# Kernel tuning notes

Measured on AMD Instinct MI355X. Metric: run time of the kernel, lower is better.

Reference implementation:

```python
import jax, jax.numpy as jnp
import numpy as np

N_NODES = 100_000
N_EDGES = 1_600_000
F_IN = 32
F_OUT = 32
DIM = 2
K = 5                      # kernel_size per dim (open spline)
KTOT = K ** DIM            # 25 kernel weight matrices
S = 2 ** DIM               # 4 nonzero linear-B-spline basis terms per edge
NEG_SLOPE = 0.2

# offsets over the 2^DIM corners of the spline cell, [S, DIM]
_OFFSETS = np.array([[(s >> d) & 1 for d in range(DIM)] for s in range(S)], dtype=np.int32)
_STRIDES = np.array([K ** d for d in range(DIM)], dtype=np.int32)


def _spline_basis(pseudo):
    """Degree-1 open B-spline basis. pseudo: [E, DIM] in [0,1].
    Returns basis [E, S] and kernel-weight indices widx [E, S]."""
    offsets = jnp.asarray(_OFFSETS)
    strides = jnp.asarray(_STRIDES)
    p = pseudo * (K - 1)                         # open spline scaling
    fl = jnp.floor(p)
    frac = p - fl                                # [E, DIM]
    b = jnp.where(offsets[None] == 0, 1.0 - frac[:, None, :], frac[:, None, :])
    basis = jnp.prod(b, axis=-1)                 # [E, S]
    idx = jnp.clip(fl.astype(jnp.int32)[:, None, :] + offsets[None], 0, K - 1)
    widx = jnp.sum(idx * strides, axis=-1)       # [E, S] in [0, KTOT)
    return basis, widx


def setup_inputs() -> dict:
    key = jax.random.key(0)
    ks = jax.random.split(key, 7)
    x = jax.random.normal(ks[0], (N_NODES, F_IN), dtype=jnp.float32)
    edge_index = jax.random.randint(ks[1], (2, N_EDGES), 0, N_NODES)
    pseudo = jax.random.uniform(ks[2], (N_EDGES, DIM), dtype=jnp.float32)
    bound = 1.0 / np.sqrt(KTOT * F_IN)           # matches reset_parameters uniform(size, ...)
    weight = jax.random.uniform(ks[3], (KTOT, F_IN, F_OUT), jnp.float32, -bound, bound)
    root_weight = jax.random.uniform(ks[4], (F_IN, F_OUT), jnp.float32, -bound, bound)
    att_weight = jax.random.uniform(ks[5], (2 * F_OUT,), jnp.float32, -bound, bound)
    bias = jax.random.uniform(ks[6], (F_OUT,), jnp.float32, -bound, bound)
    return {"x": x, "edge_index": edge_index, "pseudo": pseudo, "weight": weight,
            "root_weight": root_weight, "att_weight": att_weight, "bias": bias}


def reference(x, edge_index, pseudo, weight, root_weight, att_weight, bias):
    row, col = edge_index[0], edge_index[1]      # row = target, col = source
    basis, widx = _spline_basis(pseudo)          # [E,S], [E,S]

    # Precompute x @ W_k for every kernel weight: [N, KTOT, F_OUT]
    xw = jnp.einsum('nf,kfo->nko', x, weight)
    flat = col[:, None] * KTOT + widx            # [E, S] flat (node, kernel) index
    gathered = xw.reshape(-1, F_OUT)[flat]       # [E, S, F_OUT]
    msg = jnp.einsum('es,esf->ef', basis, gathered)  # spline-weighted edge messages

    x_root = x @ root_weight                     # [N, F_OUT]

    # GAT-style attention logits: cat([x_root[row], msg]) . att_weight
    alpha = x_root[row] @ att_weight[:F_OUT] + msg @ att_weight[F_OUT:]
    alpha = jnp.where(alpha > 0, alpha, NEG_SLOPE * alpha)  # leaky relu

    # segment softmax over incoming edges of each target node
    amax = jax.ops.segment_max(alpha, row, num_segments=N_NODES)
    amax = jnp.where(jnp.isfinite(amax), amax, 0.0)
    ex = jnp.exp(alpha - amax[row])
    denom = jax.ops.segment_sum(ex, row, num_segments=N_NODES)
    att = ex / (denom[row] + 1e-16)

    out = jax.ops.segment_sum(msg * att[:, None], row, num_segments=N_NODES)
    return out + x_root + bias
```

## Files before the change

### kernel.cpp

```cpp
#include <hip/hip_runtime.h>
#include <stdint.h>

#define N_NODES 100000
#define N_EDGES 1600000
#define NBLK_SCAN 391

typedef __attribute__((ext_vector_type(8))) short short8;
typedef __attribute__((ext_vector_type(4))) float float4v;

__device__ __forceinline__ unsigned short f32_to_bf16(float f) {
  uint32_t u = __float_as_uint(f);
  u += 0x7fffu + ((u >> 16) & 1u);
  return (unsigned short)(u >> 16);
}
__device__ __forceinline__ float bf16_to_f32(unsigned short h) {
  return __uint_as_float(((uint32_t)h) << 16);
}

__global__ __launch_bounds__(256) void k_zero(
    const float* __restrict__ weight, const float* __restrict__ root_w,
    int* __restrict__ deg, unsigned short* __restrict__ wbf) {
  int tid = threadIdx.x;
  int b = blockIdx.x;
  int i = b * 256 + tid;
  if (i < N_NODES) deg[i] = 0;
  if (b < 100) {
    int e = i;
    int t = e >> 9, rem = e & 511;
    int q = rem >> 7, row = (rem >> 3) & 15, j = rem & 7;
    int km = t >> 1, fin = q * 8 + j, fo = (t & 1) * 16 + row;
    wbf[e] = f32_to_bf16(weight[(km * 32 + fin) * 32 + fo]);
  } else if (b == 100) {
    for (int idx = tid; idx < 1024; idx += 256) {
      int t = 50 + (idx >> 9), rem = idx & 511;
      int q = rem >> 7, row = (rem >> 3) & 15, j = rem & 7;
      int fin = q * 8 + j, fo = (t - 50) * 16 + row;
      wbf[t * 512 + rem] = f32_to_bf16(root_w[fin * 32 + fo]);
    }
  }
}

__global__ __launch_bounds__(256) void k1_xw(
    const float* __restrict__ x, const unsigned short* __restrict__ wbf,
    const int* __restrict__ ei, const float* __restrict__ att_w,
    const float* __restrict__ bias,
    int* __restrict__ deg, unsigned short* __restrict__ rank,
    unsigned short* __restrict__ xw, float* __restrict__ out,
    uint2* __restrict__ od) {
  __shared__ __align__(16) uint2 st[3200];
  int tid = threadIdx.x;
  int b = blockIdx.x;

  int e = b * 256 + tid;
  int rk = atomicAdd(&deg[ei[e]], 1);

  int wave = tid >> 6, lane = tid & 63;
  int quad = lane >> 4, c16 = lane & 15;
  int n0 = b * 16;
  int node = n0 + c16;
  const float* xp = x + (size_t)node * 32 + quad * 8;
  float4 a0 = *reinterpret_cast<const float4*>(xp);
  float4 a1 = *reinterpret_cast<const float4*>(xp + 4);
  short8 af;
  af[0] = (short)f32_to_bf16(a0.x); af[1] = (short)f32_to_bf16(a0.y);
  af[2] = (short)f32_to_bf16(a0.z); af[3] = (short)f32_to_bf16(a0.w);
  af[4] = (short)f32_to_bf16(a1.x); af[5] = (short)f32_to_bf16(a1.y);
  af[6] = (short)f32_to_bf16(a1.z); af[7] = (short)f32_to_bf16(a1.w);

  float rsum = 0.f;
  for (int idx = 0; idx < 13; idx++) {
    int t = wave * 13 + idx;
    short8 bf = *reinterpret_cast<const short8*>(wbf + ((t * 4 + quad) * 16 + c16) * 8);
    float4v acc = {0.f, 0.f, 0.f, 0.f};
    acc = __builtin_amdgcn_mfma_f32_16x16x32_bf16(bf, af, acc, 0, 0, 0);
    if (t < 50) {
      uint2 pk;
      pk.x = (unsigned int)f32_to_bf16(acc[0]) |
             ((unsigned int)f32_to_bf16(acc[1]) << 16);
      pk.y = (unsigned int)f32_to_bf16(acc[2]) |
             ((unsigned int)f32_to_bf16(acc[3]) << 16);
      int tq = t * 4 + quad;
      st[tq * 16 + (c16 ^ (tq & 15))] = pk;
    } else {
      int gfo = (t - 50) * 16 + quad * 4;
      float4 bi = *reinterpret_cast<const float4*>(bias + gfo);
      float4 o;
      o.x = acc[0] + bi.x; o.y = acc[1] + bi.y;
      o.z = acc[2] + bi.z; o.w = acc[3] + bi.w;
      *reinterpret_cast<float4*>(out + (size_t)node * 32 + gfo) = o;
      float4 aw = *reinterpret_cast<const float4*>(att_w + gfo);
      rsum += acc[0] * aw.x + acc[1] * aw.y + acc[2] * aw.z + acc[3] * aw.w;
    }
  }
  if (wave == 3) {
    rsum += __shfl_xor(rsum, 16);
    rsum += __shfl_xor(rsum, 32);
    if (lane < 16) od[node].y = __float_as_uint(rsum);
  }
  __syncthreads();
  uint2* dst = reinterpret_cast<uint2*>(xw) + (size_t)n0 * 200;
  for (int j = tid; j < 3200; j += 256) {
    int nd = j / 200;
    int tq = j - nd * 200;
    dst[j] = st[tq * 16 + (nd ^ (tq & 15))];
  }
  rank[e] = (unsigned short)rk;
}

__global__ __launch_bounds__(256) void kscan1(const int* __restrict__ deg,
                                              int* __restrict__ incl,
                                              int* __restrict__ bsum) {
  __shared__ int s[256];
  int tid = threadIdx.x;
  int i = blockIdx.x * 256 + tid;
  int v = (i < N_NODES) ? deg[i] : 0;
  s[tid] = v;
  __syncthreads();
  for (int d = 1; d < 256; d <<= 1) {
    int t = (tid >= d) ? s[tid - d] : 0;
    __syncthreads();
    s[tid] += t;
    __syncthreads();
  }
  if (i < N_NODES) incl[i] = s[tid];
  if (tid == 255) bsum[blockIdx.x] = s[255];
}

__global__ __launch_bounds__(512) void kscan2(const int* __restrict__ bsum,
                                              int* __restrict__ bbase) {
  __shared__ int s[512];
  int tid = threadIdx.x;
  int v = (tid < NBLK_SCAN) ? bsum[tid] : 0;
  s[tid] = v;
  __syncthreads();
  for (int d = 1; d < 512; d <<= 1) {
    int t = (tid >= d) ? s[tid - d] : 0;
    __syncthreads();
    s[tid] += t;
    __syncthreads();
  }
  if (tid < NBLK_SCAN) bbase[tid] = s[tid] - v;
}

__global__ __launch_bounds__(256) void kscan3(const int* __restrict__ deg,
                                              int* __restrict__ offs,
                                              const int* __restrict__ bbase,
                                              uint2* __restrict__ od) {
  int i = blockIdx.x * 256 + threadIdx.x;
  if (i < N_NODES) {
    int v = offs[i] - deg[i] + bbase[i >> 8];
    offs[i] = v;
    od[i].x = (unsigned int)v;
  }
  if (i == 0) {
    offs[N_NODES] = N_EDGES;
    od[N_NODES].x = (unsigned int)N_EDGES;
  }
}

__global__ __launch_bounds__(256) void kscatter(
    const int* __restrict__ ei, const float* __restrict__ pseudo,
    const uint2* __restrict__ od, const unsigned short* __restrict__ rank,
    uint2* __restrict__ epack) {
  int e = blockIdx.x * 256 + threadIdx.x;
  int r = ei[e];
  int c = ei[N_EDGES + e];
  float p0 = pseudo[2 * e] * 4.f;
  float p1 = pseudo[2 * e + 1] * 4.f;
  int rk = rank[e];
  unsigned int offr = od[r].x;
  float fl0 = floorf(p0), fl1 = floorf(p1);
  float fr0 = p0 - fl0, fr1 = p1 - fl1;
  int i0 = (int)fl0, i1 = (int)fl1;
  int w0 = i0 + 5 * i1;
  unsigned int q0 = (unsigned int)(fr0 * 65535.f + 0.5f);
  unsigned int q1 = (unsigned int)(fr1 * 65535.f + 0.5f);
  uint2 pk;
  pk.x = (unsigned int)(c * 800 + w0 * 32);
  pk.y = q0 | (q1 << 16);
  epack[offr + rk] = pk;
}

__global__ __launch_bounds__(256) void k2_csr(
    const uint2* __restrict__ od, const uint2* __restrict__ epack,
    const unsigned short* __restrict__ xw, const float* __restrict__ att_w,
    float* __restrict__ out) {
  int tid = threadIdx.x;
  int wave = tid >> 6, lane = tid & 63;
  int node = blockIdx.x * 4 + wave;
  if (node >= N_NODES) return;
  int f = lane & 31, half = lane >> 5;
  uint2 v0 = od[node];
  int s0 = (int)v0.x;
  int s1 = (int)od[node + 1].x;
  float rd = __uint_as_float(v0.y);
  float a2 = att_w[32 + f];
  const unsigned short* xwf = xw + f;
  float acc = 0.f, den = 0.f;
  int i = s0 + half;
  const float Q = 1.f / 65535.f;

  for (; i + 6 < s1; i += 8) {
    uint2 p[4];
    p[0] = epack[i];     p[1] = epack[i + 2];
    p[2] = epack[i + 4]; p[3] = epack[i + 6];
    float fr0[4], fr1[4];
#pragma unroll
    for (int u = 0; u < 4; u++) {
      fr0[u] = (float)(p[u].y & 0xffff) * Q;
      fr1[u] = (float)(p[u].y >> 16) * Q;
    }
    float g0[4], g1[4], g2[4], g3[4];
#pragma unroll
    for (int u = 0; u < 4; u++) {
      const unsigned short* base = xwf + p[u].x;
      g0[u] = bf16_to_f32(base[0]);
      g1[u] = bf16_to_f32(base[32]);
      g2[u] = bf16_to_f32(base[160]);
      g3[u] = bf16_to_f32(base[192]);
    }
    float msg[4], t[4];
#pragma unroll
    for (int u = 0; u < 4; u++) {
      float c0 = 1.f - fr0[u], c1 = 1.f - fr1[u];
      msg[u] = c1 * (c0 * g0[u] + fr0[u] * g1[u]) +
               fr1[u] * (c0 * g2[u] + fr0[u] * g3[u]);
      t[u] = msg[u] * a2;
    }
#pragma unroll
    for (int m = 16; m >= 1; m >>= 1) {
      t[0] += __shfl_xor(t[0], m);
      t[1] += __shfl_xor(t[1], m);
      t[2] += __shfl_xor(t[2], m);
      t[3] += __shfl_xor(t[3], m);
    }
#pragma unroll
    for (int u = 0; u < 4; u++) {
      float alpha = rd + t[u];
      alpha = alpha > 0.f ? alpha : 0.2f * alpha;
      float ex = __expf(alpha);
      acc += msg[u] * ex;
      den += ex;
    }
  }
  for (; i < s1; i += 2) {
    uint2 pv = epack[i];
    float fr0 = (float)(pv.y & 0xffff) * Q;
    float fr1 = (float)(pv.y >> 16) * Q;
    const unsigned short* base = xwf + pv.x;
    float g0 = bf16_to_f32(base[0]);
    float g1 = bf16_to_f32(base[32]);
    float g2 = bf16_to_f32(base[160]);
    float g3 = bf16_to_f32(base[192]);
    float c0 = 1.f - fr0, c1 = 1.f - fr1;
    float msg = c1 * (c0 * g0 + fr0 * g1) + fr1 * (c0 * g2 + fr0 * g3);
    float t = msg * a2;
#pragma unroll
    for (int m = 16; m >= 1; m >>= 1) t += __shfl_xor(t, m);
    float alpha = rd + t;
    alpha = alpha > 0.f ? alpha : 0.2f * alpha;
    float ex = __expf(alpha);
    acc += msg * ex;
    den += ex;
  }

  acc += __shfl_xor(acc, 32);
  den += __shfl_xor(den, 32);
  if (half == 0) out[node * 32 + f] += acc / (den + 1e-16f);
}

extern "C" void kernel_launch(void* const* d_in, const int* in_sizes, int n_in,
                              void* d_out, int out_size, void* d_ws, size_t ws_size,
                              hipStream_t stream) {
  const float* x      = (const float*)d_in[0];
  const int*   ei     = (const int*)d_in[1];
  const float* pseudo = (const float*)d_in[2];
  const float* weight = (const float*)d_in[3];
  const float* root_w = (const float*)d_in[4];
  const float* att_w  = (const float*)d_in[5];
  const float* bias   = (const float*)d_in[6];
  float* out = (float*)d_out;

  char* ws = (char*)d_ws;
  unsigned short* xw   = (unsigned short*)ws;
  uint2* od            = (uint2*)(ws + 160000000);
  unsigned short* wbf  = (unsigned short*)(ws + 160800016);
  int* deg             = (int*)(ws + 160853264);
  int* offs            = (int*)(ws + 161253264);
  int* bsum            = (int*)(ws + 161653280);
  int* bbase           = (int*)(ws + 161654880);
  unsigned short* rank = (unsigned short*)(ws + 161656480);
  uint2* epack         = (uint2*)(ws + 164856480);

  hipLaunchKernelGGL(k_zero, dim3(NBLK_SCAN), dim3(256), 0, stream,
                     weight, root_w, deg, wbf);
  hipLaunchKernelGGL(k1_xw, dim3(6250), dim3(256), 0, stream,
                     x, wbf, ei, att_w, bias, deg, rank, xw, out, od);
  hipLaunchKernelGGL(kscan1, dim3(NBLK_SCAN), dim3(256), 0, stream, deg, offs, bsum);
  hipLaunchKernelGGL(kscan2, dim3(1), dim3(512), 0, stream, bsum, bbase);
  hipLaunchKernelGGL(kscan3, dim3(NBLK_SCAN), dim3(256), 0, stream,
                     deg, offs, bbase, od);
  hipLaunchKernelGGL(kscatter, dim3(6250), dim3(256), 0, stream,
                     ei, pseudo, od, rank, epack);
  hipLaunchKernelGGL(k2_csr, dim3(25000), dim3(256), 0, stream,
                     od, epack, xw, att_w, out);
}
```

Measured before the change: 325.2 us.

## Compute spline messages per edge with MFMA instead of precomputing x@W for all kernels

The per-node precompute of x@W_k for all 25 kernels (a 160MB bf16 table) is replaced by storing bf16 x only. Messages are computed on the fly in the CSR kernel: 16 edges per wave gather source rows, and MFMAs run against the kernel weights staged in LDS, skipped when no lane needs that kernel. The aim is to cut the large xw write and the scattered gather traffic. In exchange the edge kernel does far more MFMA work, since divergent kernel indices across 16 edges can trigger most of the 25 weight pairs.

```diff
diff --git a/kernel.cpp b/kernel.cpp
--- a/kernel.cpp
+++ b/kernel.cpp
@@ -12,9 +12,6 @@
   uint32_t u = __float_as_uint(f);
   u += 0x7fffu + ((u >> 16) & 1u);
   return (unsigned short)(u >> 16);
-}
-__device__ __forceinline__ float bf16_to_f32(unsigned short h) {
-  return __uint_as_float(((uint32_t)h) << 16);
 }
 
 __global__ __launch_bounds__(256) void k_zero(
@@ -40,14 +37,13 @@
   }
 }
 
-__global__ __launch_bounds__(256) void k1_xw(
+__global__ __launch_bounds__(256) void k1_lite(
     const float* __restrict__ x, const unsigned short* __restrict__ wbf,
     const int* __restrict__ ei, const float* __restrict__ att_w,
     const float* __restrict__ bias,
     int* __restrict__ deg, unsigned short* __restrict__ rank,
-    unsigned short* __restrict__ xw, float* __restrict__ out,
+    unsigned short* __restrict__ xb, float* __restrict__ out,
     uint2* __restrict__ od) {
-  __shared__ __align__(16) uint2 st[3200];
   int tid = threadIdx.x;
   int b = blockIdx.x;
 
@@ -56,8 +52,7 @@
 
   int wave = tid >> 6, lane = tid & 63;
   int quad = lane >> 4, c16 = lane & 15;
-  int n0 = b * 16;
-  int node = n0 + c16;
+  int node = b * 16 + c16;
   const float* xp = x + (size_t)node * 32 + quad * 8;
   float4 a0 = *reinterpret_cast<const float4*>(xp);
   float4 a1 = *reinterpret_cast<const float4*>(xp + 4);
@@ -67,21 +62,16 @@
   af[4] = (short)f32_to_bf16(a1.x); af[5] = (short)f32_to_bf16(a1.y);
   af[6] = (short)f32_to_bf16(a1.z); af[7] = (short)f32_to_bf16(a1.w);
 
-  float rsum = 0.f;
-  for (int idx = 0; idx < 13; idx++) {
-    int t = wave * 13 + idx;
-    short8 bf = *reinterpret_cast<const short8*>(wbf + ((t * 4 + quad) * 16 + c16) * 8);
-    float4v acc = {0.f, 0.f, 0.f, 0.f};
-    acc = __builtin_amdgcn_mfma_f32_16x16x32_bf16(bf, af, acc, 0, 0, 0);
-    if (t < 50) {
-      uint2 pk;
-      pk.x = (unsigned int)f32_to_bf16(acc[0]) |
-             ((unsigned int)f32_to_bf16(acc[1]) << 16);
-      pk.y = (unsigned int)f32_to_bf16(acc[2]) |
-             ((unsigned int)f32_to_bf16(acc[3]) << 16);
-      int tq = t * 4 + quad;
-      st[tq * 16 + (c16 ^ (tq & 15))] = pk;
-    } else {
+  if (wave == 0) {
+    *reinterpret_cast<short8*>(xb + (size_t)node * 32 + quad * 8) = af;
+  }
+  if (wave == 3) {
+    float rsum = 0.f;
+#pragma unroll
+    for (int t = 50; t <= 51; t++) {
+      short8 bf = *reinterpret_cast<const short8*>(wbf + ((t * 4 + quad) * 16 + c16) * 8);
+      float4v acc = {0.f, 0.f, 0.f, 0.f};
+      acc = __builtin_amdgcn_mfma_f32_16x16x32_bf16(bf, af, acc, 0, 0, 0);
       int gfo = (t - 50) * 16 + quad * 4;
       float4 bi = *reinterpret_cast<const float4*>(bias + gfo);
       float4 o;
@@ -91,18 +81,9 @@
       float4 aw = *reinterpret_cast<const float4*>(att_w + gfo);
       rsum += acc[0] * aw.x + acc[1] * aw.y + acc[2] * aw.z + acc[3] * aw.w;
     }
-  }
-  if (wave == 3) {
     rsum += __shfl_xor(rsum, 16);
     rsum += __shfl_xor(rsum, 32);
     if (lane < 16) od[node].y = __float_as_uint(rsum);
-  }
-  __syncthreads();
-  uint2* dst = reinterpret_cast<uint2*>(xw) + (size_t)n0 * 200;
-  for (int j = tid; j < 3200; j += 256) {
-    int nd = j / 200;
-    int tq = j - nd * 200;
-    dst[j] = st[tq * 16 + (nd ^ (tq & 15))];
   }
   rank[e] = (unsigned short)rk;
 }
@@ -176,97 +157,117 @@
   unsigned int q0 = (unsigned int)(fr0 * 65535.f + 0.5f);
   unsigned int q1 = (unsigned int)(fr1 * 65535.f + 0.5f);
   uint2 pk;
-  pk.x = (unsigned int)(c * 800 + w0 * 32);
+  pk.x = (unsigned int)c | ((unsigned int)w0 << 17);
   pk.y = q0 | (q1 << 16);
   epack[offr + rk] = pk;
 }
 
-__global__ __launch_bounds__(256) void k2_csr(
+__global__ __launch_bounds__(512) void k2_fused(
     const uint2* __restrict__ od, const uint2* __restrict__ epack,
-    const unsigned short* __restrict__ xw, const float* __restrict__ att_w,
-    float* __restrict__ out) {
-  int tid = threadIdx.x;
+    const unsigned short* __restrict__ xb, const unsigned short* __restrict__ wbf,
+    const float* __restrict__ att_w, float* __restrict__ out) {
+  __shared__ __align__(16) unsigned short lw[25600];
+  int tid = threadIdx.x;
+  {
+    const uint4* src = reinterpret_cast<const uint4*>(wbf);
+    uint4* dst = reinterpret_cast<uint4*>(lw);
+    for (int j = tid; j < 3200; j += 512) dst[j] = src[j];
+  }
+  __syncthreads();
+
   int wave = tid >> 6, lane = tid & 63;
-  int node = blockIdx.x * 4 + wave;
-  if (node >= N_NODES) return;
-  int f = lane & 31, half = lane >> 5;
+  int quad = lane >> 4, c16 = lane & 15;
+  int node = blockIdx.x * 8 + wave;
   uint2 v0 = od[node];
   int s0 = (int)v0.x;
   int s1 = (int)od[node + 1].x;
   float rd = __uint_as_float(v0.y);
-  float a2 = att_w[32 + f];
-  const unsigned short* xwf = xw + f;
-  float acc = 0.f, den = 0.f;
-  int i = s0 + half;
+
+  float aw0[4], aw1[4];
+#pragma unroll
+  for (int r = 0; r < 4; r++) {
+    aw0[r] = att_w[32 + quad * 4 + r];
+    aw1[r] = att_w[48 + quad * 4 + r];
+  }
+
+  float acc0[4] = {0.f, 0.f, 0.f, 0.f};
+  float acc1[4] = {0.f, 0.f, 0.f, 0.f};
+  float den = 0.f;
   const float Q = 1.f / 65535.f;
 
-  for (; i + 6 < s1; i += 8) {
-    uint2 p[4];
-    p[0] = epack[i];     p[1] = epack[i + 2];
-    p[2] = epack[i + 4]; p[3] = epack[i + 6];
-    float fr0[4], fr1[4];
-#pragma unroll
-    for (int u = 0; u < 4; u++) {
-      fr0[u] = (float)(p[u].y & 0xffff) * Q;
-      fr1[u] = (float)(p[u].y >> 16) * Q;
-    }
-    float g0[4], g1[4], g2[4], g3[4];
-#pragma unroll
-    for (int u = 0; u < 4; u++) {
-      const unsigned short* base = xwf + p[u].x;
-      g0[u] = bf16_to_f32(base[0]);
-      g1[u] = bf16_to_f32(base[32]);
-      g2[u] = bf16_to_f32(base[160]);
-      g3[u] = bf16_to_f32(base[192]);
-    }
-    float msg[4], t[4];
-#pragma unroll
-    for (int u = 0; u < 4; u++) {
-      float c0 = 1.f - fr0[u], c1 = 1.f - fr1[u];
-      msg[u] = c1 * (c0 * g0[u] + fr0[u] * g1[u]) +
-               fr1[u] * (c0 * g2[u] + fr0[u] * g3[u]);
-      t[u] = msg[u] * a2;
-    }
-#pragma unroll
-    for (int m = 16; m >= 1; m >>= 1) {
-      t[0] += __shfl_xor(t[0], m);
-      t[1] += __shfl_xor(t[1], m);
-      t[2] += __shfl_xor(t[2], m);
-      t[3] += __shfl_xor(t[3], m);
-    }
-#pragma unroll
-    for (int u = 0; u < 4; u++) {
-      float alpha = rd + t[u];
-      alpha = alpha > 0.f ? alpha : 0.2f * alpha;
-      float ex = __expf(alpha);
-      acc += msg[u] * ex;
-      den += ex;
-    }
-  }
-  for (; i < s1; i += 2) {
-    uint2 pv = epack[i];
-    float fr0 = (float)(pv.y & 0xffff) * Q;
-    float fr1 = (float)(pv.y >> 16) * Q;
-    const unsigned short* base = xwf + pv.x;
-    float g0 = bf16_to_f32(base[0]);
-    float g1 = bf16_to_f32(base[32]);
-    float g2 = bf16_to_f32(base[160]);
-    float g3 = bf16_to_f32(base[192]);
-    float c0 = 1.f - fr0, c1 = 1.f - fr1;
-    float msg = c1 * (c0 * g0 + fr0 * g1) + fr1 * (c0 * g2 + fr0 * g3);
-    float t = msg * a2;
-#pragma unroll
-    for (int m = 16; m >= 1; m >>= 1) t += __shfl_xor(t, m);
-    float alpha = rd + t;
+  for (int base = s0; base < s1; base += 16) {
+    int m2 = s1 - base; if (m2 > 16) m2 = 16;
+    int valid = (c16 < m2);
+    uint2 ep = epack[base + (valid ? c16 : 0)];
+    int col = (int)(ep.x & 0x1FFFF);
+    int w0 = (int)(ep.x >> 17);
+    float fr0 = (float)(ep.y & 0xffff) * Q;
+    float fr1 = (float)(ep.y >> 16) * Q;
+    float b0 = (1.f - fr0) * (1.f - fr1);
+    float b1 = fr0 * (1.f - fr1);
+    float b2 = (1.f - fr0) * fr1;
+    float b3 = fr0 * fr1;
+    short8 bx = *reinterpret_cast<const short8*>(xb + (size_t)col * 32 + quad * 8);
+
+    float m0[4] = {0.f, 0.f, 0.f, 0.f};
+    float m1[4] = {0.f, 0.f, 0.f, 0.f};
+#pragma unroll
+    for (int w = 0; w < 25; w++) {
+      int dw = w - w0;
+      float cf = (dw == 0) ? b0 : (dw == 1) ? b1 : (dw == 5) ? b2
+                 : (dw == 6) ? b3 : 0.f;
+      if (__any(cf != 0.f)) {
+        short8 a0 = *reinterpret_cast<const short8*>(lw + (2 * w) * 512 + quad * 128 + c16 * 8);
+        short8 a1 = *reinterpret_cast<const short8*>(lw + (2 * w + 1) * 512 + quad * 128 + c16 * 8);
+        float4v z0 = {0.f, 0.f, 0.f, 0.f};
+        float4v z1 = {0.f, 0.f, 0.f, 0.f};
+        z0 = __builtin_amdgcn_mfma_f32_16x16x32_bf16(a0, bx, z0, 0, 0, 0);
+        z1 = __builtin_amdgcn_mfma_f32_16x16x32_bf16(a1, bx, z1, 0, 0, 0);
+#pragma unroll
+        for (int r = 0; r < 4; r++) {
+          m0[r] += cf * z0[r];
+          m1[r] += cf * z1[r];
+        }
+      }
+    }
+    float p = 0.f;
+#pragma unroll
+    for (int r = 0; r < 4; r++) p += m0[r] * aw0[r] + m1[r] * aw1[r];
+    p += __shfl_xor(p, 16);
+    p += __shfl_xor(p, 32);
+    float alpha = rd + p;
     alpha = alpha > 0.f ? alpha : 0.2f * alpha;
-    float ex = __expf(alpha);
-    acc += msg * ex;
+    float ex = valid ? __expf(alpha) : 0.f;
     den += ex;
-  }
-
-  acc += __shfl_xor(acc, 32);
-  den += __shfl_xor(den, 32);
-  if (half == 0) out[node * 32 + f] += acc / (den + 1e-16f);
+#pragma unroll
+    for (int r = 0; r < 4; r++) {
+      acc0[r] += ex * m0[r];
+      acc1[r] += ex * m1[r];
+    }
+  }
+
+#pragma unroll
+  for (int msk = 1; msk <= 8; msk <<= 1) {
+    den += __shfl_xor(den, msk);
+#pragma unroll
+    for (int r = 0; r < 4; r++) {
+      acc0[r] += __shfl_xor(acc0[r], msk);
+      acc1[r] += __shfl_xor(acc1[r], msk);
+    }
+  }
+  if (c16 == 0) {
+    float inv = 1.f / (den + 1e-16f);
+    float* op = out + (size_t)node * 32 + quad * 4;
+    float4 o0 = *reinterpret_cast<const float4*>(op);
+    o0.x += acc0[0] * inv; o0.y += acc0[1] * inv;
+    o0.z += acc0[2] * inv; o0.w += acc0[3] * inv;
+    *reinterpret_cast<float4*>(op) = o0;
+    float* op1 = op + 16;
+    float4 o1 = *reinterpret_cast<const float4*>(op1);
+    o1.x += acc1[0] * inv; o1.y += acc1[1] * inv;
+    o1.z += acc1[2] * inv; o1.w += acc1[3] * inv;
+    *reinterpret_cast<float4*>(op1) = o1;
+  }
 }
 
 extern "C" void kernel_launch(void* const* d_in, const int* in_sizes, int n_in,
@@ -282,26 +283,26 @@
   float* out = (float*)d_out;
 
   char* ws = (char*)d_ws;
-  unsigned short* xw   = (unsigned short*)ws;
-  uint2* od            = (uint2*)(ws + 160000000);
-  unsigned short* wbf  = (unsigned short*)(ws + 160800016);
-  int* deg             = (int*)(ws + 160853264);
-  int* offs            = (int*)(ws + 161253264);
-  int* bsum            = (int*)(ws + 161653280);
-  int* bbase           = (int*)(ws + 161654880);
-  unsigned short* rank = (unsigned short*)(ws + 161656480);
-  uint2* epack         = (uint2*)(ws + 164856480);
+  unsigned short* xb   = (unsigned short*)ws;
+  uint2* od            = (uint2*)(ws + 6400000);
+  unsigned short* wbf  = (unsigned short*)(ws + 7200016);
+  int* deg             = (int*)(ws + 7253264);
+  int* offs            = (int*)(ws + 7653264);
+  int* bsum            = (int*)(ws + 8053280);
+  int* bbase           = (int*)(ws + 8054880);
+  unsigned short* rank = (unsigned short*)(ws + 8056480);
+  uint2* epack         = (uint2*)(ws + 11256480);
 
   hipLaunchKernelGGL(k_zero, dim3(NBLK_SCAN), dim3(256), 0, stream,
                      weight, root_w, deg, wbf);
-  hipLaunchKernelGGL(k1_xw, dim3(6250), dim3(256), 0, stream,
-                     x, wbf, ei, att_w, bias, deg, rank, xw, out, od);
+  hipLaunchKernelGGL(k1_lite, dim3(6250), dim3(256), 0, stream,
+                     x, wbf, ei, att_w, bias, deg, rank, xb, out, od);
   hipLaunchKernelGGL(kscan1, dim3(NBLK_SCAN), dim3(256), 0, stream, deg, offs, bsum);
   hipLaunchKernelGGL(kscan2, dim3(1), dim3(512), 0, stream, bsum, bbase);
   hipLaunchKernelGGL(kscan3, dim3(NBLK_SCAN), dim3(256), 0, stream,
                      deg, offs, bbase, od);
   hipLaunchKernelGGL(kscatter, dim3(6250), dim3(256), 0, stream,
                      ei, pseudo, od, rank, epack);
-  hipLaunchKernelGGL(k2_csr, dim3(25000), dim3(256), 0, stream,
-                     od, epack, xw, att_w, out);
-}
+  hipLaunchKernelGGL(k2_fused, dim3(12500), dim3(512), 0, stream,
+                     od, epack, xb, wbf, att_w, out);
+}
```

Measured after the change: 430.3 us. 1.32x slower.

## Fuse three scan kernels into one with last-block decoupled reduction

Applied to the files above, without the earlier changes.

Merges the three-kernel prefix scan into a single kernel. Each block writes its local inclusive sum and degree, and the last block to finish (found with an atomic counter) scans the block totals. Final offsets are no longer materialised; the scatter and CSR kernels rebuild them from the local inclusive value, the degree and the block base. This removes two kernel launches and one full pass over the degree array, in exchange for a threadfence and atomic handshake and a few extra loads in the downstream kernels.

```diff
diff --git a/kernel.cpp b/kernel.cpp
--- a/kernel.cpp
+++ b/kernel.cpp
@@ -19,7 +19,8 @@
 
 __global__ __launch_bounds__(256) void k_zero(
     const float* __restrict__ weight, const float* __restrict__ root_w,
-    int* __restrict__ deg, unsigned short* __restrict__ wbf) {
+    int* __restrict__ deg, unsigned short* __restrict__ wbf,
+    int* __restrict__ done) {
   int tid = threadIdx.x;
   int b = blockIdx.x;
   int i = b * 256 + tid;
@@ -37,6 +38,8 @@
       int fin = q * 8 + j, fo = (t - 50) * 16 + row;
       wbf[t * 512 + rem] = f32_to_bf16(root_w[fin * 32 + fo]);
     }
+  } else if (b == 101) {
+    if (tid == 0) done[0] = 0;
   }
 }
 
@@ -46,7 +49,7 @@
     const float* __restrict__ bias,
     int* __restrict__ deg, unsigned short* __restrict__ rank,
     unsigned short* __restrict__ xw, float* __restrict__ out,
-    uint2* __restrict__ od) {
+    float* __restrict__ r_dot) {
   __shared__ __align__(16) uint2 st[3200];
   int tid = threadIdx.x;
   int b = blockIdx.x;
@@ -95,7 +98,7 @@
   if (wave == 3) {
     rsum += __shfl_xor(rsum, 16);
     rsum += __shfl_xor(rsum, 32);
-    if (lane < 16) od[node].y = __float_as_uint(rsum);
+    if (lane < 16) r_dot[node] = rsum;
   }
   __syncthreads();
   uint2* dst = reinterpret_cast<uint2*>(xw) + (size_t)n0 * 200;
@@ -107,12 +110,14 @@
   rank[e] = (unsigned short)rk;
 }
 
-__global__ __launch_bounds__(256) void kscan1(const int* __restrict__ deg,
-                                              int* __restrict__ incl,
-                                              int* __restrict__ bsum) {
+__global__ __launch_bounds__(256) void kscan1m(
+    const int* __restrict__ deg, uint2* __restrict__ id2,
+    int* __restrict__ bsum, int* __restrict__ bbase, int* __restrict__ done) {
   __shared__ int s[256];
+  __shared__ int islast;
   int tid = threadIdx.x;
-  int i = blockIdx.x * 256 + tid;
+  int b = blockIdx.x;
+  int i = b * 256 + tid;
   int v = (i < N_NODES) ? deg[i] : 0;
   s[tid] = v;
   __syncthreads();
@@ -122,53 +127,58 @@
     s[tid] += t;
     __syncthreads();
   }
-  if (i < N_NODES) incl[i] = s[tid];
-  if (tid == 255) bsum[blockIdx.x] = s[255];
-}
-
-__global__ __launch_bounds__(512) void kscan2(const int* __restrict__ bsum,
-                                              int* __restrict__ bbase) {
-  __shared__ int s[512];
-  int tid = threadIdx.x;
-  int v = (tid < NBLK_SCAN) ? bsum[tid] : 0;
-  s[tid] = v;
-  __syncthreads();
-  for (int d = 1; d < 512; d <<= 1) {
+  if (i < N_NODES) {
+    uint2 pk; pk.x = (unsigned int)s[tid]; pk.y = (unsigned int)v;
+    id2[i] = pk;
+  }
+  if (tid == 255) bsum[b] = s[255];
+  __syncthreads();
+  if (tid == 0) {
+    __threadfence();
+    islast = (atomicAdd(done, 1) == NBLK_SCAN - 1);
+  }
+  __syncthreads();
+  if (!islast) return;
+  int v0 = __hip_atomic_load(&bsum[tid], __ATOMIC_RELAXED,
+                             __HIP_MEMORY_SCOPE_AGENT);
+  s[tid] = v0;
+  __syncthreads();
+  for (int d = 1; d < 256; d <<= 1) {
     int t = (tid >= d) ? s[tid - d] : 0;
     __syncthreads();
     s[tid] += t;
     __syncthreads();
   }
-  if (tid < NBLK_SCAN) bbase[tid] = s[tid] - v;
-}
-
-__global__ __launch_bounds__(256) void kscan3(const int* __restrict__ deg,
-                                              int* __restrict__ offs,
-                                              const int* __restrict__ bbase,
-                                              uint2* __restrict__ od) {
-  int i = blockIdx.x * 256 + threadIdx.x;
-  if (i < N_NODES) {
-    int v = offs[i] - deg[i] + bbase[i >> 8];
-    offs[i] = v;
-    od[i].x = (unsigned int)v;
-  }
-  if (i == 0) {
-    offs[N_NODES] = N_EDGES;
-    od[N_NODES].x = (unsigned int)N_EDGES;
-  }
+  bbase[tid] = s[tid] - v0;
+  int carry = s[255];
+  __syncthreads();
+  int v1 = (tid < NBLK_SCAN - 256)
+               ? __hip_atomic_load(&bsum[256 + tid], __ATOMIC_RELAXED,
+                                   __HIP_MEMORY_SCOPE_AGENT)
+               : 0;
+  s[tid] = v1;
+  __syncthreads();
+  for (int d = 1; d < 256; d <<= 1) {
+    int t = (tid >= d) ? s[tid - d] : 0;
+    __syncthreads();
+    s[tid] += t;
+    __syncthreads();
+  }
+  if (tid < NBLK_SCAN - 256) bbase[256 + tid] = carry + s[tid] - v1;
 }
 
 __global__ __launch_bounds__(256) void kscatter(
     const int* __restrict__ ei, const float* __restrict__ pseudo,
-    const uint2* __restrict__ od, const unsigned short* __restrict__ rank,
-    uint2* __restrict__ epack) {
+    const uint2* __restrict__ id2, const int* __restrict__ bbase,
+    const unsigned short* __restrict__ rank, uint2* __restrict__ epack) {
   int e = blockIdx.x * 256 + threadIdx.x;
   int r = ei[e];
   int c = ei[N_EDGES + e];
   float p0 = pseudo[2 * e] * 4.f;
   float p1 = pseudo[2 * e + 1] * 4.f;
   int rk = rank[e];
-  unsigned int offr = od[r].x;
+  uint2 idv = id2[r];
+  int pos = (int)idv.x - (int)idv.y + bbase[r >> 8] + rk;
   float fl0 = floorf(p0), fl1 = floorf(p1);
   float fr0 = p0 - fl0, fr1 = p1 - fl1;
   int i0 = (int)fl0, i1 = (int)fl1;
@@ -178,11 +188,12 @@
   uint2 pk;
   pk.x = (unsigned int)(c * 800 + w0 * 32);
   pk.y = q0 | (q1 << 16);
-  epack[offr + rk] = pk;
+  epack[pos] = pk;
 }
 
 __global__ __launch_bounds__(256) void k2_csr(
-    const uint2* __restrict__ od, const uint2* __restrict__ epack,
+    const uint2* __restrict__ id2, const int* __restrict__ bbase,
+    const float* __restrict__ r_dot, const uint2* __restrict__ epack,
     const unsigned short* __restrict__ xw, const float* __restrict__ att_w,
     float* __restrict__ out) {
   int tid = threadIdx.x;
@@ -190,10 +201,10 @@
   int node = blockIdx.x * 4 + wave;
   if (node >= N_NODES) return;
   int f = lane & 31, half = lane >> 5;
-  uint2 v0 = od[node];
-  int s0 = (int)v0.x;
-  int s1 = (int)od[node + 1].x;
-  float rd = __uint_as_float(v0.y);
+  uint2 v0 = id2[node];
+  int s1 = (int)v0.x + bbase[node >> 8];
+  int s0 = s1 - (int)v0.y;
+  float rd = r_dot[node];
   float a2 = att_w[32 + f];
   const unsigned short* xwf = xw + f;
   float acc = 0.f, den = 0.f;
@@ -283,25 +294,24 @@
 
   char* ws = (char*)d_ws;
   unsigned short* xw   = (unsigned short*)ws;
-  uint2* od            = (uint2*)(ws + 160000000);
-  unsigned short* wbf  = (unsigned short*)(ws + 160800016);
-  int* deg             = (int*)(ws + 160853264);
-  int* offs            = (int*)(ws + 161253264);
-  int* bsum            = (int*)(ws + 161653280);
-  int* bbase           = (int*)(ws + 161654880);
-  unsigned short* rank = (unsigned short*)(ws + 161656480);
-  uint2* epack         = (uint2*)(ws + 164856480);
+  float* r_dot         = (float*)(ws + 160000000);
+  unsigned short* wbf  = (unsigned short*)(ws + 160400000);
+  int* deg             = (int*)(ws + 160453248);
+  uint2* id2           = (uint2*)(ws + 160853248);
+  int* bsum            = (int*)(ws + 161653248);
+  int* bbase           = (int*)(ws + 161654848);
+  int* done            = (int*)(ws + 161656448);
+  unsigned short* rank = (unsigned short*)(ws + 161656464);
+  uint2* epack         = (uint2*)(ws + 164856464);
 
   hipLaunchKernelGGL(k_zero, dim3(NBLK_SCAN), dim3(256), 0, stream,
-                     weight, root_w, deg, wbf);
+                     weight, root_w, deg, wbf, done);
   hipLaunchKernelGGL(k1_xw, dim3(6250), dim3(256), 0, stream,
-                     x, wbf, ei, att_w, bias, deg, rank, xw, out, od);
-  hipLaunchKernelGGL(kscan1, dim3(NBLK_SCAN), dim3(256), 0, stream, deg, offs, bsum);
-  hipLaunchKernelGGL(kscan2, dim3(1), dim3(512), 0, stream, bsum, bbase);
-  hipLaunchKernelGGL(kscan3, dim3(NBLK_SCAN), dim3(256), 0, stream,
-                     deg, offs, bbase, od);
+                     x, wbf, ei, att_w, bias, deg, rank, xw, out, r_dot);
+  hipLaunchKernelGGL(kscan1m, dim3(NBLK_SCAN), dim3(256), 0, stream,
+                     deg, id2, bsum, bbase, done);
   hipLaunchKernelGGL(kscatter, dim3(6250), dim3(256), 0, stream,
-                     ei, pseudo, od, rank, epack);
+                     ei, pseudo, id2, bbase, rank, epack);
   hipLaunchKernelGGL(k2_csr, dim3(25000), dim3(256), 0, stream,
-                     od, epack, xw, att_w, out);
-}
+                     id2, bbase, r_dot, epack, xw, att_w, out);
+}
```

After: 328.0 us. Within noise of the previous version (+0.9%).
